# Performance work log

Hardware: AMD Instinct MI355X
Metric: run time of the kernel (lower is better)

Reference implementation:

```python
import jax, jax.numpy as jnp
import numpy as np

L, E, NH, V, BS = 8, 1024, 16, 32000, 1024  # layers, embed, heads, vocab, block_size
HD = E // NH  # head dim = 64
FF = 4 * E


def layernorm(x, scale, bias, eps=1e-5):
    mu = jnp.mean(x, axis=-1, keepdims=True)
    var = jnp.var(x, axis=-1, keepdims=True)
    return (x - mu) * jax.lax.rsqrt(var + eps) * scale + bias


def setup_inputs() -> dict:
    key = jax.random.key(0)
    ks = jax.random.split(key, 16)
    s = 0.02
    B, T = 2, 1024
    return {
        "idx": jax.random.randint(ks[0], (B, T), 0, V),
        "tok_emb": jax.random.normal(ks[1], (V, E), jnp.float32) * s,
        "pos_emb": jax.random.normal(ks[2], (BS, E), jnp.float32) * s,
        "Wq": jax.random.normal(ks[3], (L, E, E), jnp.float32) * s,
        "Wk": jax.random.normal(ks[4], (L, E, E), jnp.float32) * s,
        "Wv": jax.random.normal(ks[5], (L, E, E), jnp.float32) * s,
        "Wo": jax.random.normal(ks[6], (L, E, E), jnp.float32) * s,
        "bo": jnp.zeros((L, E), jnp.float32),
        "ln1_s": jnp.ones((L, E), jnp.float32),
        "ln1_b": jnp.zeros((L, E), jnp.float32),
        "W1": jax.random.normal(ks[7], (L, E, FF), jnp.float32) * s,
        "b1": jnp.zeros((L, FF), jnp.float32),
        "W2": jax.random.normal(ks[8], (L, FF, E), jnp.float32) * s,
        "b2": jnp.zeros((L, E), jnp.float32),
        "ln2_s": jnp.ones((L, E), jnp.float32),
        "ln2_b": jnp.zeros((L, E), jnp.float32),
        "lnf_s": jnp.ones((E,), jnp.float32),
        "lnf_b": jnp.zeros((E,), jnp.float32),
        "lm_w": jax.random.normal(ks[9], (E, V), jnp.float32) * s,
        "lm_b": jnp.zeros((V,), jnp.float32),
    }


def reference(idx, tok_emb, pos_emb, Wq, Wk, Wv, Wo, bo, ln1_s, ln1_b,
              W1, b1, W2, b2, ln2_s, ln2_b, lnf_s, lnf_b, lm_w, lm_b):
    B, T = idx.shape
    x = tok_emb[idx] + pos_emb[:T]  # [B,T,E]
    causal = jnp.triu(jnp.ones((T, T), bool), 1)  # True above diagonal -> masked
    scale = 1.0 / jnp.sqrt(jnp.asarray(HD, x.dtype))
    for l in range(L):
        h = layernorm(x, ln1_s[l], ln1_b[l])
        q = (h @ Wq[l]).reshape(B, T, NH, HD)
        k = (h @ Wk[l]).reshape(B, T, NH, HD)
        v = (h @ Wv[l]).reshape(B, T, NH, HD)
        scores = jnp.einsum("bthd,bshd->bhts", q, k) * scale  # [B,H,T,T]
        scores = jnp.where(causal, -jnp.inf, scores)
        attn = jax.nn.softmax(scores, axis=-1)
        o = jnp.einsum("bhts,bshd->bthd", attn, v).reshape(B, T, E)
        x = x + o @ Wo[l] + bo[l]
        h2 = layernorm(x, ln2_s[l], ln2_b[l])
        x = x + jax.nn.gelu(h2 @ W1[l] + b1[l], approximate=False) @ W2[l] + b2[l]
    x = layernorm(x, lnf_s, lnf_b)
    logits = x @ lm_w + lm_b  # [B,T,V]
    return logits
```

## Files before the change

### kernel.cpp

```cpp
#include <hip/hip_runtime.h>

#define EDIM 1024
#define NHEADS 16
#define HDIM 64
#define TSEQ 1024
#define NBATCH 2
#define MROWS 2048
#define FFDIM 4096
#define NLAYERS 8
#define VOCAB 32000
#define QKVN 3072
#define SC2 0.18033688011112042f

typedef __attribute__((ext_vector_type(4))) float f32x4;
typedef __attribute__((ext_vector_type(8))) short short8;

__device__ __forceinline__ unsigned short f2bf(float f) {
    union { float f; unsigned u; } v; v.f = f;
    unsigned r = v.u + 0x7fffu + ((v.u >> 16) & 1u);
    return (unsigned short)(r >> 16);
}

__device__ __forceinline__ f32x4 mfma_bf16(short8 a, short8 b, f32x4 c) {
    return __builtin_amdgcn_mfma_f32_16x16x32_bf16(a, b, c, 0, 0, 0);
}

__device__ __forceinline__ void gload16(const unsigned short* g, unsigned short* l) {
    __builtin_amdgcn_global_load_lds(
        (const __attribute__((address_space(1))) unsigned int*)g,
        (__attribute__((address_space(3))) unsigned int*)l, 16, 0, 0);
}

__global__ __launch_bounds__(256) void embed_kernel(
    const int* __restrict__ idx, const float* __restrict__ tok,
    const float* __restrict__ pos, float* __restrict__ x)
{
    int row = blockIdx.x;
    int t = row & (TSEQ - 1);
    int tokid = idx[row];
    const float* tp = tok + (size_t)tokid * EDIM;
    const float* pp = pos + (size_t)t * EDIM;
    float* xp = x + (size_t)row * EDIM;
    int c = threadIdx.x * 4;
    f32x4 a = *(const f32x4*)(tp + c);
    f32x4 b = *(const f32x4*)(pp + c);
    *(f32x4*)(xp + c) = a + b;
}

__device__ __forceinline__ void ln_store(
    f32x4 v, int tid, const float* __restrict__ sc, const float* __restrict__ bi,
    unsigned short* __restrict__ hrow)
{
    float sum = v[0] + v[1] + v[2] + v[3];
    float sq = v[0]*v[0] + v[1]*v[1] + v[2]*v[2] + v[3]*v[3];
    #pragma unroll
    for (int m = 1; m <= 32; m <<= 1) { sum += __shfl_xor(sum, m); sq += __shfl_xor(sq, m); }
    __shared__ float sh[8];
    int w = tid >> 6;
    if ((tid & 63) == 0) { sh[w] = sum; sh[4 + w] = sq; }
    __syncthreads();
    sum = sh[0] + sh[1] + sh[2] + sh[3];
    sq  = sh[4] + sh[5] + sh[6] + sh[7];
    float mu = sum * (1.0f / EDIM);
    float inv = rsqrtf(sq * (1.0f / EDIM) - mu * mu + 1e-5f);
    int c = tid * 4;
    unsigned o0 = (unsigned)f2bf((v[0] - mu) * inv * sc[c + 0] + bi[c + 0])
                | ((unsigned)f2bf((v[1] - mu) * inv * sc[c + 1] + bi[c + 1]) << 16);
    unsigned o1 = (unsigned)f2bf((v[2] - mu) * inv * sc[c + 2] + bi[c + 2])
                | ((unsigned)f2bf((v[3] - mu) * inv * sc[c + 3] + bi[c + 3]) << 16);
    unsigned* hp = (unsigned*)(hrow + c);
    hp[0] = o0; hp[1] = o1;
}

__global__ __launch_bounds__(256) void ln_kernel(
    const float* __restrict__ x, const float* __restrict__ sc,
    const float* __restrict__ bi, unsigned short* __restrict__ h)
{
    int row = blockIdx.x, tid = threadIdx.x;
    f32x4 v = *(const f32x4*)(x + (size_t)row * EDIM + tid * 4);
    ln_store(v, tid, sc, bi, h + (size_t)row * EDIM);
}

template<int KZ>
__global__ __launch_bounds__(256) void reduce_ln_kernel(
    const float* __restrict__ part, const float* __restrict__ bias,
    float* __restrict__ x, const float* __restrict__ sc,
    const float* __restrict__ bi, unsigned short* __restrict__ h)
{
    int row = blockIdx.x, tid = threadIdx.x;
    int c = tid * 4;
    f32x4 s = *(const f32x4*)(x + (size_t)row * EDIM + c);
    s += *(const f32x4*)(bias + c);
    #pragma unroll
    for (int kz = 0; kz < KZ; ++kz)
        s += *(const f32x4*)(part + ((size_t)kz * MROWS + row) * EDIM + c);
    *(f32x4*)(x + (size_t)row * EDIM + c) = s;
    ln_store(s, tid, sc, bi, h + (size_t)row * EDIM);
}

__device__ __forceinline__ void conv_tile(
    const float* __restrict__ W, unsigned short* __restrict__ WT,
    int Kdim, int Ndim, int k0, int n0, int tid)
{
    __shared__ unsigned short T[64][72];
    int r = tid >> 4, c4 = (tid & 15) * 4;
    #pragma unroll
    for (int i = 0; i < 4; ++i) {
        f32x4 v = *(const f32x4*)(W + (size_t)(k0 + r + 16 * i) * Ndim + n0 + c4);
        T[c4 + 0][r + 16 * i] = f2bf(v[0]);
        T[c4 + 1][r + 16 * i] = f2bf(v[1]);
        T[c4 + 2][r + 16 * i] = f2bf(v[2]);
        T[c4 + 3][r + 16 * i] = f2bf(v[3]);
    }
    __syncthreads();
    int nr = tid >> 2, kc = (tid & 3) * 16;
    short8 o0 = *(const short8*)&T[nr][kc];
    short8 o1 = *(const short8*)&T[nr][kc + 8];
    *(short8*)(WT + (size_t)(n0 + nr) * Kdim + k0 + kc)     = o0;
    *(short8*)(WT + (size_t)(n0 + nr) * Kdim + k0 + kc + 8) = o1;
}

__global__ __launch_bounds__(256) void wconv_layer_kernel(
    const float* __restrict__ Wq, const float* __restrict__ Wk,
    const float* __restrict__ Wv, const float* __restrict__ Wo,
    const float* __restrict__ W1, const float* __restrict__ W2,
    unsigned short* __restrict__ qkvT, unsigned short* __restrict__ woT,
    unsigned short* __restrict__ w1T, unsigned short* __restrict__ w2T)
{
    int bid = blockIdx.x, tid = threadIdx.x;
    if (bid < 768) {
        int wsel = bid >> 8, t = bid & 255;
        const float* src = wsel == 0 ? Wq : (wsel == 1 ? Wk : Wv);
        conv_tile(src, qkvT + (size_t)wsel * EDIM * EDIM, EDIM, EDIM,
                  (t & 15) * 64, (t >> 4) * 64, tid);
    } else if (bid < 1024) {
        int t = bid - 768;
        conv_tile(Wo, woT, EDIM, EDIM, (t & 15) * 64, (t >> 4) * 64, tid);
    } else if (bid < 2048) {
        int t = bid - 1024;
        conv_tile(W1, w1T, EDIM, FFDIM, (t & 15) * 64, (t >> 4) * 64, tid);
    } else {
        int t = bid - 2048;
        conv_tile(W2, w2T, FFDIM, EDIM, (t >> 4) * 64, (t & 15) * 64, tid);
    }
}

__global__ __launch_bounds__(256) void wconv_kernel(
    const float* __restrict__ W, unsigned short* __restrict__ WT, int Kdim, int Ndim)
{
    conv_tile(W, WT, Kdim, Ndim, blockIdx.x * 64, blockIdx.y * 64, threadIdx.x);
}

template<int EPI>
__global__ __launch_bounds__(256, 3) void gemm128(
    const unsigned short* __restrict__ A, const unsigned short* __restrict__ WT,
    const float* __restrict__ bias, float* __restrict__ Cf,
    unsigned short* __restrict__ Cb, int Ndim, int Kdim,
    int ntiles, int nwg, int kspan)
{
    __shared__ __align__(16) unsigned short A_lds[128][64];
    __shared__ __align__(16) unsigned short B_lds[128][64];
    int tid = threadIdx.x;
    int q8 = nwg >> 3;
    int swz = (int)(blockIdx.x & 7) * q8 + (int)(blockIdx.x >> 3);
    int bm0 = (swz / ntiles) * 128, bn0 = (swz % ntiles) * 128;
    int kz = blockIdx.y;
    int lane = tid & 63, w = tid >> 6;
    int wr = w >> 1, wc = w & 1;
    int r16 = lane & 15, cc = lane >> 4;
    int lrow = lane >> 3;
    int lcol = ((lane & 7) ^ lrow) * 8;
    int sw = r16 & 7;

    f32x4 acc[4][4];
    #pragma unroll
    for (int m = 0; m < 4; ++m)
        #pragma unroll
        for (int n = 0; n < 4; ++n) acc[m][n] = {0.f, 0.f, 0.f, 0.f};

    int kbeg = kz * kspan, kend = kbeg + kspan;
    for (int k0 = kbeg; k0 < kend; k0 += 64) {
        #pragma unroll
        for (int i = 0; i < 4; ++i) {
            int c = i * 4 + w;
            gload16(A + (size_t)(bm0 + c * 8 + lrow) * Kdim + k0 + lcol,
                    (unsigned short*)A_lds + c * 512);
            gload16(WT + (size_t)(bn0 + c * 8 + lrow) * Kdim + k0 + lcol,
                    (unsigned short*)B_lds + c * 512);
        }
        __syncthreads();
        #pragma unroll
        for (int kh = 0; kh < 2; ++kh) {
            short8 af[4], bfr[4];
            #pragma unroll
            for (int m = 0; m < 4; ++m)
                af[m] = *(const short8*)&A_lds[wr * 64 + m * 16 + r16][((kh * 4 + cc) ^ sw) * 8];
            #pragma unroll
            for (int n = 0; n < 4; ++n)
                bfr[n] = *(const short8*)&B_lds[wc * 64 + n * 16 + r16][((kh * 4 + cc) ^ sw) * 8];
            #pragma unroll
            for (int m = 0; m < 4; ++m)
                #pragma unroll
                for (int n = 0; n < 4; ++n)
                    acc[m][n] = mfma_bf16(af[m], bfr[n], acc[m][n]);
        }
        __syncthreads();
    }

    #pragma unroll
    for (int m = 0; m < 4; ++m) {
        #pragma unroll
        for (int n = 0; n < 4; ++n) {
            #pragma unroll
            for (int j = 0; j < 4; ++j) {
                int row = bm0 + wr * 64 + m * 16 + cc * 4 + j;
                int col = bn0 + wc * 64 + n * 16 + r16;
                float vv = acc[m][n][j];
                if constexpr (EPI == 0)
                    Cb[(size_t)row * Ndim + col] = f2bf(vv);
                else
                    (Cf + (size_t)kz * MROWS * Ndim)[(size_t)row * Ndim + col] = vv;
            }
        }
    }
}

template<int EPI>
__global__ __launch_bounds__(512, 2) void gemm_p3(
    const unsigned short* __restrict__ A, const unsigned short* __restrict__ WT,
    const float* __restrict__ bias, float* __restrict__ Cf,
    unsigned short* __restrict__ Cb, int Ndim, int Kdim, int mtiles, int ntiles)
{
    __shared__ __align__(16) unsigned short LDS[3][24576];
    const int tid = threadIdx.x;
    const int nwg = mtiles * ntiles, q8 = nwg >> 3;
    const int swz = (int)(blockIdx.x & 7) * q8 + (int)(blockIdx.x >> 3);
    const int bn0 = (swz / mtiles) * 256, bm0 = (swz % mtiles) * 128;
    const int lane = tid & 63, w = tid >> 6;
    const int wr = w >> 2, wc = w & 3;
    const int r16 = lane & 15, cc = lane >> 4;
    const int lrow = lane >> 3;
    const int lcol = ((lane & 7) ^ lrow) * 8;
    const int sw = r16 & 7;

    f32x4 acc[4][4];
    #pragma unroll
    for (int m = 0; m < 4; ++m)
        #pragma unroll
        for (int n = 0; n < 4; ++n) acc[m][n] = {0.f, 0.f, 0.f, 0.f};

    const int nk = Kdim >> 6;

    auto STAGE = [&](int t, int bufidx) {
        int k0 = t * 64;
        unsigned short* buf = &LDS[bufidx][0];
        #pragma unroll
        for (int i = 0; i < 2; ++i) {
            int c = i * 8 + w;
            gload16(A + (size_t)(bm0 + c * 8 + lrow) * Kdim + k0 + lcol, buf + c * 512);
        }
        #pragma unroll
        for (int i = 0; i < 4; ++i) {
            int c = i * 8 + w;
            gload16(WT + (size_t)(bn0 + c * 8 + lrow) * Kdim + k0 + lcol, buf + 8192 + c * 512);
        }
    };

    STAGE(0, 0);
    STAGE(1, 1);
    asm volatile("s_waitcnt vmcnt(6)" ::: "memory");
    __builtin_amdgcn_sched_barrier(0);
    __builtin_amdgcn_s_barrier();
    __builtin_amdgcn_sched_barrier(0);

    int cur = 0;
    for (int t = 0; t < nk; ++t) {
        if (t + 2 < nk) STAGE(t + 2, cur == 0 ? 2 : cur - 1);
        const unsigned short* Abuf = &LDS[cur][0];
        const unsigned short* Bbuf = &LDS[cur][8192];
        #pragma unroll
        for (int kh = 0; kh < 2; ++kh) {
            short8 af[4], bfr[4];
            #pragma unroll
            for (int m = 0; m < 4; ++m)
                af[m] = *(const short8*)&Abuf[(wr * 64 + m * 16 + r16) * 64 + ((kh * 4 + cc) ^ sw) * 8];
            #pragma unroll
            for (int n = 0; n < 4; ++n)
                bfr[n] = *(const short8*)&Bbuf[(wc * 64 + n * 16 + r16) * 64 + ((kh * 4 + cc) ^ sw) * 8];
            __builtin_amdgcn_s_setprio(1);
            #pragma unroll
            for (int m = 0; m < 4; ++m)
                #pragma unroll
                for (int n = 0; n < 4; ++n)
                    acc[m][n] = mfma_bf16(af[m], bfr[n], acc[m][n]);
            __builtin_amdgcn_s_setprio(0);
        }
        if (t + 1 < nk) {
            if (t + 2 < nk) asm volatile("s_waitcnt vmcnt(6)" ::: "memory");
            else            asm volatile("s_waitcnt vmcnt(0)" ::: "memory");
            __builtin_amdgcn_sched_barrier(0);
            __builtin_amdgcn_s_barrier();
            __builtin_amdgcn_sched_barrier(0);
            asm volatile("" ::: "memory");
        }
        cur = cur == 2 ? 0 : cur + 1;
    }

    #pragma unroll
    for (int m = 0; m < 4; ++m) {
        #pragma unroll
        for (int n = 0; n < 4; ++n) {
            #pragma unroll
            for (int j = 0; j < 4; ++j) {
                int row = bm0 + wr * 64 + m * 16 + cc * 4 + j;
                int col = bn0 + wc * 64 + n * 16 + r16;
                float vv = acc[m][n][j] + bias[col];
                if constexpr (EPI == 2) {
                    vv = 0.5f * vv * (1.0f + erff(vv * 0.70710678118654752f));
                    Cb[(size_t)row * Ndim + col] = f2bf(vv);
                } else {
                    Cf[(size_t)row * Ndim + col] = vv;
                }
            }
        }
    }
}

__global__ __launch_bounds__(256, 2) void gemm_wide_lm(
    const unsigned short* __restrict__ A, const unsigned short* __restrict__ WT,
    const float* __restrict__ bias, float* __restrict__ Cf,
    int Ndim, int Kdim, int mtiles, int ntiles)
{
    __shared__ __align__(16) unsigned short A_lds[128][64];
    __shared__ __align__(16) unsigned short B_lds[256][64];
    int tid = threadIdx.x;
    int nwg = mtiles * ntiles;
    int q8 = nwg >> 3;
    int swz = (int)(blockIdx.x & 7) * q8 + (int)(blockIdx.x >> 3);
    int bn0 = (swz / mtiles) * 256, bm0 = (swz % mtiles) * 128;
    int lane = tid & 63, w = tid >> 6;
    int wr = w >> 1, wc = w & 1;
    int r16 = lane & 15, cc = lane >> 4;
    int lrow = lane >> 3;
    int lcol = ((lane & 7) ^ lrow) * 8;
    int sw = r16 & 7;

    f32x4 acc[4][8];
    #pragma unroll
    for (int m = 0; m < 4; ++m)
        #pragma unroll
        for (int n = 0; n < 8; ++n) acc[m][n] = {0.f, 0.f, 0.f, 0.f};

    for (int k0 = 0; k0 < Kdim; k0 += 64) {
        #pragma unroll
        for (int i = 0; i < 4; ++i) {
            int c = i * 4 + w;
            gload16(A + (size_t)(bm0 + c * 8 + lrow) * Kdim + k0 + lcol,
                    (unsigned short*)A_lds + c * 512);
        }
        #pragma unroll
        for (int i = 0; i < 8; ++i) {
            int c = i * 4 + w;
            gload16(WT + (size_t)(bn0 + c * 8 + lrow) * Kdim + k0 + lcol,
                    (unsigned short*)B_lds + c * 512);
        }
        __syncthreads();
        #pragma unroll
        for (int kh = 0; kh < 2; ++kh) {
            short8 af[4], bfr[8];
            #pragma unroll
            for (int m = 0; m < 4; ++m)
                af[m] = *(const short8*)&A_lds[wr * 64 + m * 16 + r16][((kh * 4 + cc) ^ sw) * 8];
            #pragma unroll
            for (int n = 0; n < 8; ++n)
                bfr[n] = *(const short8*)&B_lds[wc * 128 + n * 16 + r16][((kh * 4 + cc) ^ sw) * 8];
            #pragma unroll
            for (int m = 0; m < 4; ++m)
                #pragma unroll
                for (int n = 0; n < 8; ++n)
                    acc[m][n] = mfma_bf16(af[m], bfr[n], acc[m][n]);
        }
        __syncthreads();
    }

    #pragma unroll
    for (int m = 0; m < 4; ++m) {
        #pragma unroll
        for (int n = 0; n < 8; ++n) {
            #pragma unroll
            for (int j = 0; j < 4; ++j) {
                int row = bm0 + wr * 64 + m * 16 + cc * 4 + j;
                int col = bn0 + wc * 128 + n * 16 + r16;
                Cf[(size_t)row * Ndim + col] = acc[m][n][j] + bias[col];
            }
        }
    }
}

__global__ __launch_bounds__(256) void attn_kernel(
    const unsigned short* __restrict__ qkv, unsigned short* __restrict__ o)
{
    __shared__ __align__(16) unsigned short K_lds[128][72];
    __shared__ __align__(16) unsigned short VT_lds[64][136];
    __shared__ __align__(16) unsigned short P_lds[4][16][136];

    int qt = blockIdx.x, head = blockIdx.y, bb = blockIdx.z;
    int tid = threadIdx.x, w = tid >> 6, lane = tid & 63;
    int r16 = lane & 15, cc = lane >> 4;
    size_t base = ((size_t)bb * TSEQ) * QKVN + head * HDIM;
    const unsigned short* q = qkv + base;
    const unsigned short* k = qkv + base + EDIM;
    const unsigned short* v = qkv + base + 2 * EDIM;
    size_t obase = ((size_t)bb * TSEQ) * EDIM + head * HDIM;
    int qbase = qt * 64;

    const unsigned short* qp = q + (size_t)(qbase + w * 16 + r16) * QKVN;
    short8 aq0 = *(const short8*)(qp + cc * 8);
    short8 aq1 = *(const short8*)(qp + 32 + cc * 8);

    f32x4 oacc[4];
    float m2[4], lrow[4];
    #pragma unroll
    for (int n = 0; n < 4; ++n) oacc[n] = {0.f, 0.f, 0.f, 0.f};
    #pragma unroll
    for (int j = 0; j < 4; ++j) { m2[j] = -1e30f; lrow[j] = 0.f; }

    int krow = tid >> 1, kch = (tid & 1) * 32;
    int vk2 = (tid & 63) * 2, vdb = (tid >> 6) * 16;

    int nkt = (qt + 2) >> 1;
    for (int kt = 0; kt < nkt; ++kt) {
        int kbase = kt * 128;
        const unsigned short* kp = k + (size_t)(kbase + krow) * QKVN + kch;
        *(short8*)&K_lds[krow][kch]      = *(const short8*)kp;
        *(short8*)&K_lds[krow][kch + 8]  = *(const short8*)(kp + 8);
        *(short8*)&K_lds[krow][kch + 16] = *(const short8*)(kp + 16);
        *(short8*)&K_lds[krow][kch + 24] = *(const short8*)(kp + 24);
        const unsigned short* vp0 = v + (size_t)(kbase + vk2) * QKVN + vdb;
        short8 v0a = *(const short8*)vp0;
        short8 v0b = *(const short8*)(vp0 + 8);
        short8 v1a = *(const short8*)(vp0 + QKVN);
        short8 v1b = *(const short8*)(vp0 + QKVN + 8);
        #pragma unroll
        for (int i = 0; i < 8; ++i) {
            *(unsigned*)&VT_lds[vdb + i][vk2] =
                (unsigned)(unsigned short)v0a[i] | ((unsigned)(unsigned short)v1a[i] << 16);
            *(unsigned*)&VT_lds[vdb + 8 + i][vk2] =
                (unsigned)(unsigned short)v0b[i] | ((unsigned)(unsigned short)v1b[i] << 16);
        }
        __syncthreads();

        f32x4 s[8];
        __builtin_amdgcn_s_setprio(1);
        #pragma unroll
        for (int n = 0; n < 8; ++n) {
            short8 bk0 = *(const short8*)&K_lds[n * 16 + r16][cc * 8];
            short8 bk1 = *(const short8*)&K_lds[n * 16 + r16][32 + cc * 8];
            f32x4 z = {0.f, 0.f, 0.f, 0.f};
            z = mfma_bf16(aq0, bk0, z);
            z = mfma_bf16(aq1, bk1, z);
            s[n] = z;
        }
        __builtin_amdgcn_s_setprio(0);
        int myrow = qbase + w * 16 + cc * 4;
        #pragma unroll
        for (int n = 0; n < 8; ++n) {
            int key = kbase + n * 16 + r16;
            #pragma unroll
            for (int j = 0; j < 4; ++j) {
                float sv = s[n][j] * SC2;
                if (key > myrow + j) sv = -1e30f;
                s[n][j] = sv;
            }
        }
        float tmax[4];
        #pragma unroll
        for (int j = 0; j < 4; ++j) {
            float t0 = fmaxf(fmaxf(s[0][j], s[1][j]), fmaxf(s[2][j], s[3][j]));
            float t1 = fmaxf(fmaxf(s[4][j], s[5][j]), fmaxf(s[6][j], s[7][j]));
            float tm = fmaxf(t0, t1);
            #pragma unroll
            for (int mm = 1; mm <= 8; mm <<= 1) tm = fmaxf(tm, __shfl_xor(tm, mm));
            tmax[j] = tm;
        }
        bool defer = (tmax[0] - m2[0] <= 11.5f) && (tmax[1] - m2[1] <= 11.5f)
                  && (tmax[2] - m2[2] <= 11.5f) && (tmax[3] - m2[3] <= 11.5f);
        if (!__all(defer)) {
            #pragma unroll
            for (int j = 0; j < 4; ++j) {
                float mnew = fmaxf(m2[j], tmax[j]);
                float al = exp2f(m2[j] - mnew);
                m2[j] = mnew;
                lrow[j] *= al;
                #pragma unroll
                for (int n = 0; n < 4; ++n) oacc[n][j] *= al;
            }
        }
        #pragma unroll
        for (int j = 0; j < 4; ++j) {
            float ts = 0.f;
            #pragma unroll
            for (int n = 0; n < 8; ++n) {
                float pe = exp2f(s[n][j] - m2[j]);
                s[n][j] = pe;
                ts += pe;
            }
            #pragma unroll
            for (int mm = 1; mm <= 8; mm <<= 1) ts += __shfl_xor(ts, mm);
            lrow[j] += ts;
        }
        #pragma unroll
        for (int n = 0; n < 8; ++n)
            #pragma unroll
            for (int j = 0; j < 4; ++j)
                P_lds[w][cc * 4 + j][n * 16 + r16] = f2bf(s[n][j]);
        short8 pa[4];
        #pragma unroll
        for (int qq = 0; qq < 4; ++qq)
            pa[qq] = *(const short8*)&P_lds[w][r16][qq * 32 + cc * 8];
        __builtin_amdgcn_s_setprio(1);
        #pragma unroll
        for (int n = 0; n < 4; ++n) {
            #pragma unroll
            for (int qq = 0; qq < 4; ++qq) {
                short8 bv = *(const short8*)&VT_lds[n * 16 + r16][qq * 32 + cc * 8];
                oacc[n] = mfma_bf16(pa[qq], bv, oacc[n]);
            }
        }
        __builtin_amdgcn_s_setprio(0);
        __syncthreads();
    }
    float rl[4];
    #pragma unroll
    for (int j = 0; j < 4; ++j) rl[j] = 1.0f / lrow[j];
    #pragma unroll
    for (int n = 0; n < 4; ++n)
        #pragma unroll
        for (int j = 0; j < 4; ++j) {
            int row = qbase + w * 16 + cc * 4 + j;
            o[obase + (size_t)row * EDIM + n * 16 + r16] = f2bf(oacc[n][j] * rl[j]);
        }
}

extern "C" void kernel_launch(void* const* d_in, const int* in_sizes, int n_in,
                              void* d_out, int out_size, void* d_ws, size_t ws_size,
                              hipStream_t stream) {
    const int*   idx     = (const int*)d_in[0];
    const float* tok_emb = (const float*)d_in[1];
    const float* pos_emb = (const float*)d_in[2];
    const float* Wq      = (const float*)d_in[3];
    const float* Wk      = (const float*)d_in[4];
    const float* Wv      = (const float*)d_in[5];
    const float* Wo      = (const float*)d_in[6];
    const float* bo      = (const float*)d_in[7];
    const float* ln1_s   = (const float*)d_in[8];
    const float* ln1_b   = (const float*)d_in[9];
    const float* W1      = (const float*)d_in[10];
    const float* b1      = (const float*)d_in[11];
    const float* W2      = (const float*)d_in[12];
    const float* b2      = (const float*)d_in[13];
    const float* ln2_s   = (const float*)d_in[14];
    const float* ln2_b   = (const float*)d_in[15];
    const float* lnf_s   = (const float*)d_in[16];
    const float* lnf_b   = (const float*)d_in[17];
    const float* lm_w    = (const float*)d_in[18];
    const float* lm_b    = (const float*)d_in[19];
    float* out = (float*)d_out;

    char* ws = (char*)d_ws;
    float*          x    = (float*)ws;
    unsigned short* h    = (unsigned short*)(ws + (8  << 20));
    unsigned short* qkv  = (unsigned short*)(ws + (12 << 20));
    unsigned short* ao   = (unsigned short*)(ws + (24 << 20));
    unsigned short* ff   = (unsigned short*)(ws + (28 << 20));
    unsigned short* qkvT = (unsigned short*)(ws + (44 << 20));
    unsigned short* woT  = (unsigned short*)(ws + (50 << 20));
    unsigned short* w1T  = (unsigned short*)(ws + (52 << 20));
    unsigned short* w2T  = (unsigned short*)(ws + (60 << 20));
    unsigned short* lmT  = (unsigned short*)(ws + (68 << 20));
    float*          part = (float*)(ws + (68 << 20));

    dim3 blk(256);
    embed_kernel<<<MROWS, blk, 0, stream>>>(idx, tok_emb, pos_emb, x);
    ln_kernel<<<MROWS, blk, 0, stream>>>(x, ln1_s, ln1_b, h);

    for (int l = 0; l < NLAYERS; ++l) {
        size_t eo = (size_t)l * EDIM * EDIM;
        wconv_layer_kernel<<<3072, blk, 0, stream>>>(
            Wq + eo, Wk + eo, Wv + eo, Wo + eo,
            W1 + (size_t)l * EDIM * FFDIM, W2 + (size_t)l * FFDIM * EDIM,
            qkvT, woT, w1T, w2T);

        gemm128<0><<<dim3(384, 1), blk, 0, stream>>>(h, qkvT, nullptr, nullptr, qkv, QKVN, EDIM, 24, 384, EDIM);
        attn_kernel<<<dim3(TSEQ / 64, NHEADS, NBATCH), blk, 0, stream>>>(qkv, ao);
        gemm128<4><<<dim3(128, 4), blk, 0, stream>>>(ao, woT, nullptr, part, nullptr, EDIM, EDIM, 8, 128, 256);
        reduce_ln_kernel<4><<<MROWS, blk, 0, stream>>>(part, bo + l * EDIM, x, ln2_s + l * EDIM, ln2_b + l * EDIM, h);
        gemm_p3<2><<<dim3(256, 1), dim3(512), 0, stream>>>(h, w1T, b1 + l * FFDIM, nullptr, ff, FFDIM, EDIM, 16, 16);
        gemm128<4><<<dim3(128, 4), blk, 0, stream>>>(ff, w2T, nullptr, part, nullptr, EDIM, FFDIM, 8, 128, 1024);
        if (l < NLAYERS - 1)
            reduce_ln_kernel<4><<<MROWS, blk, 0, stream>>>(part, b2 + l * EDIM, x, ln1_s + (l + 1) * EDIM, ln1_b + (l + 1) * EDIM, h);
        else
            reduce_ln_kernel<4><<<MROWS, blk, 0, stream>>>(part, b2 + l * EDIM, x, lnf_s, lnf_b, h);
    }
    wconv_kernel<<<dim3(16, 500), blk, 0, stream>>>(lm_w, lmT, EDIM, VOCAB);
    gemm_wide_lm<<<dim3(2000, 1), blk, 0, stream>>>(h, lmT, lm_b, out, VOCAB, EDIM, 16, 125);
}
```

Measured before the change: 1.521 ms.

## Overlap next-layer weight conversion with FF2 GEMM in fused kernel

Merges next-layer weight conversion (and, on the last layer, the LM-head weight conversion) into the FF2 GEMM launch as extra workgroups. The conversion work then fills idle compute units instead of running as a separate serial kernel. W2 is double-buffered so the weight in use is never overwritten. Also fuses embedding with the first layernorm and reverses the attention query-tile order so the longer causal tiles are scheduled first. This needs a larger workspace, checked at runtime, and falls back to the old path otherwise.

```diff
diff --git a/kernel.cpp b/kernel.cpp
--- a/kernel.cpp
+++ b/kernel.cpp
@@ -29,22 +29,6 @@
     __builtin_amdgcn_global_load_lds(
         (const __attribute__((address_space(1))) unsigned int*)g,
         (__attribute__((address_space(3))) unsigned int*)l, 16, 0, 0);
-}
-
-__global__ __launch_bounds__(256) void embed_kernel(
-    const int* __restrict__ idx, const float* __restrict__ tok,
-    const float* __restrict__ pos, float* __restrict__ x)
-{
-    int row = blockIdx.x;
-    int t = row & (TSEQ - 1);
-    int tokid = idx[row];
-    const float* tp = tok + (size_t)tokid * EDIM;
-    const float* pp = pos + (size_t)t * EDIM;
-    float* xp = x + (size_t)row * EDIM;
-    int c = threadIdx.x * 4;
-    f32x4 a = *(const f32x4*)(tp + c);
-    f32x4 b = *(const f32x4*)(pp + c);
-    *(f32x4*)(xp + c) = a + b;
 }
 
 __device__ __forceinline__ void ln_store(
@@ -72,12 +56,20 @@
     hp[0] = o0; hp[1] = o1;
 }
 
-__global__ __launch_bounds__(256) void ln_kernel(
-    const float* __restrict__ x, const float* __restrict__ sc,
-    const float* __restrict__ bi, unsigned short* __restrict__ h)
+__global__ __launch_bounds__(256) void embed_ln_kernel(
+    const int* __restrict__ idx, const float* __restrict__ tok,
+    const float* __restrict__ pos, float* __restrict__ x,
+    const float* __restrict__ sc, const float* __restrict__ bi,
+    unsigned short* __restrict__ h)
 {
     int row = blockIdx.x, tid = threadIdx.x;
-    f32x4 v = *(const f32x4*)(x + (size_t)row * EDIM + tid * 4);
+    int t = row & (TSEQ - 1);
+    int tokid = idx[row];
+    int c = tid * 4;
+    f32x4 a = *(const f32x4*)(tok + (size_t)tokid * EDIM + c);
+    f32x4 b = *(const f32x4*)(pos + (size_t)t * EDIM + c);
+    f32x4 v = a + b;
+    *(f32x4*)(x + (size_t)row * EDIM + c) = v;
     ln_store(v, tid, sc, bi, h + (size_t)row * EDIM);
 }
 
@@ -99,25 +91,49 @@
 }
 
 __device__ __forceinline__ void conv_tile(
+    unsigned short* __restrict__ Tb,
     const float* __restrict__ W, unsigned short* __restrict__ WT,
     int Kdim, int Ndim, int k0, int n0, int tid)
 {
-    __shared__ unsigned short T[64][72];
     int r = tid >> 4, c4 = (tid & 15) * 4;
     #pragma unroll
     for (int i = 0; i < 4; ++i) {
         f32x4 v = *(const f32x4*)(W + (size_t)(k0 + r + 16 * i) * Ndim + n0 + c4);
-        T[c4 + 0][r + 16 * i] = f2bf(v[0]);
-        T[c4 + 1][r + 16 * i] = f2bf(v[1]);
-        T[c4 + 2][r + 16 * i] = f2bf(v[2]);
-        T[c4 + 3][r + 16 * i] = f2bf(v[3]);
+        Tb[(c4 + 0) * 72 + r + 16 * i] = f2bf(v[0]);
+        Tb[(c4 + 1) * 72 + r + 16 * i] = f2bf(v[1]);
+        Tb[(c4 + 2) * 72 + r + 16 * i] = f2bf(v[2]);
+        Tb[(c4 + 3) * 72 + r + 16 * i] = f2bf(v[3]);
     }
     __syncthreads();
     int nr = tid >> 2, kc = (tid & 3) * 16;
-    short8 o0 = *(const short8*)&T[nr][kc];
-    short8 o1 = *(const short8*)&T[nr][kc + 8];
+    short8 o0 = *(const short8*)&Tb[nr * 72 + kc];
+    short8 o1 = *(const short8*)&Tb[nr * 72 + kc + 8];
     *(short8*)(WT + (size_t)(n0 + nr) * Kdim + k0 + kc)     = o0;
     *(short8*)(WT + (size_t)(n0 + nr) * Kdim + k0 + kc + 8) = o1;
+}
+
+__device__ __forceinline__ void wconv_layer_body(
+    unsigned short* Tb, int t, int tid,
+    const float* Wq, const float* Wk, const float* Wv, const float* Wo,
+    const float* W1, const float* W2,
+    unsigned short* qkvT, unsigned short* woT,
+    unsigned short* w1T, unsigned short* w2T)
+{
+    if (t < 768) {
+        int wsel = t >> 8, tt = t & 255;
+        const float* src = wsel == 0 ? Wq : (wsel == 1 ? Wk : Wv);
+        conv_tile(Tb, src, qkvT + (size_t)wsel * EDIM * EDIM, EDIM, EDIM,
+                  (tt & 15) * 64, (tt >> 4) * 64, tid);
+    } else if (t < 1024) {
+        int tt = t - 768;
+        conv_tile(Tb, Wo, woT, EDIM, EDIM, (tt & 15) * 64, (tt >> 4) * 64, tid);
+    } else if (t < 2048) {
+        int tt = t - 1024;
+        conv_tile(Tb, W1, w1T, EDIM, FFDIM, (tt & 15) * 64, (tt >> 4) * 64, tid);
+    } else {
+        int tt = t - 2048;
+        conv_tile(Tb, W2, w2T, FFDIM, EDIM, (tt >> 4) * 64, (tt & 15) * 64, tid);
+    }
 }
 
 __global__ __launch_bounds__(256) void wconv_layer_kernel(
@@ -127,44 +143,31 @@
     unsigned short* __restrict__ qkvT, unsigned short* __restrict__ woT,
     unsigned short* __restrict__ w1T, unsigned short* __restrict__ w2T)
 {
-    int bid = blockIdx.x, tid = threadIdx.x;
-    if (bid < 768) {
-        int wsel = bid >> 8, t = bid & 255;
-        const float* src = wsel == 0 ? Wq : (wsel == 1 ? Wk : Wv);
-        conv_tile(src, qkvT + (size_t)wsel * EDIM * EDIM, EDIM, EDIM,
-                  (t & 15) * 64, (t >> 4) * 64, tid);
-    } else if (bid < 1024) {
-        int t = bid - 768;
-        conv_tile(Wo, woT, EDIM, EDIM, (t & 15) * 64, (t >> 4) * 64, tid);
-    } else if (bid < 2048) {
-        int t = bid - 1024;
-        conv_tile(W1, w1T, EDIM, FFDIM, (t & 15) * 64, (t >> 4) * 64, tid);
-    } else {
-        int t = bid - 2048;
-        conv_tile(W2, w2T, FFDIM, EDIM, (t >> 4) * 64, (t & 15) * 64, tid);
-    }
+    __shared__ __align__(16) unsigned short Tb[64 * 72];
+    wconv_layer_body(Tb, blockIdx.x, threadIdx.x, Wq, Wk, Wv, Wo, W1, W2,
+                     qkvT, woT, w1T, w2T);
 }
 
 __global__ __launch_bounds__(256) void wconv_kernel(
     const float* __restrict__ W, unsigned short* __restrict__ WT, int Kdim, int Ndim)
 {
-    conv_tile(W, WT, Kdim, Ndim, blockIdx.x * 64, blockIdx.y * 64, threadIdx.x);
+    __shared__ __align__(16) unsigned short Tb[64 * 72];
+    conv_tile(Tb, W, WT, Kdim, Ndim, blockIdx.x * 64, blockIdx.y * 64, threadIdx.x);
 }
 
 template<int EPI>
-__global__ __launch_bounds__(256, 3) void gemm128(
+__device__ __forceinline__ void gemm128_body(
+    unsigned short* SMEM,
     const unsigned short* __restrict__ A, const unsigned short* __restrict__ WT,
-    const float* __restrict__ bias, float* __restrict__ Cf,
-    unsigned short* __restrict__ Cb, int Ndim, int Kdim,
-    int ntiles, int nwg, int kspan)
-{
-    __shared__ __align__(16) unsigned short A_lds[128][64];
-    __shared__ __align__(16) unsigned short B_lds[128][64];
+    float* __restrict__ Cf, unsigned short* __restrict__ Cb,
+    int Ndim, int Kdim, int ntiles, int nwg, int kspan, int bid, int kz)
+{
+    unsigned short* A_lds = SMEM;
+    unsigned short* B_lds = SMEM + 8192;
     int tid = threadIdx.x;
     int q8 = nwg >> 3;
-    int swz = (int)(blockIdx.x & 7) * q8 + (int)(blockIdx.x >> 3);
+    int swz = (bid & 7) * q8 + (bid >> 3);
     int bm0 = (swz / ntiles) * 128, bn0 = (swz % ntiles) * 128;
-    int kz = blockIdx.y;
     int lane = tid & 63, w = tid >> 6;
     int wr = w >> 1, wc = w & 1;
     int r16 = lane & 15, cc = lane >> 4;
@@ -183,10 +186,8 @@
         #pragma unroll
         for (int i = 0; i < 4; ++i) {
             int c = i * 4 + w;
-            gload16(A + (size_t)(bm0 + c * 8 + lrow) * Kdim + k0 + lcol,
-                    (unsigned short*)A_lds + c * 512);
-            gload16(WT + (size_t)(bn0 + c * 8 + lrow) * Kdim + k0 + lcol,
-                    (unsigned short*)B_lds + c * 512);
+            gload16(A + (size_t)(bm0 + c * 8 + lrow) * Kdim + k0 + lcol, A_lds + c * 512);
+            gload16(WT + (size_t)(bn0 + c * 8 + lrow) * Kdim + k0 + lcol, B_lds + c * 512);
         }
         __syncthreads();
         #pragma unroll
@@ -194,10 +195,10 @@
             short8 af[4], bfr[4];
             #pragma unroll
             for (int m = 0; m < 4; ++m)
-                af[m] = *(const short8*)&A_lds[wr * 64 + m * 16 + r16][((kh * 4 + cc) ^ sw) * 8];
+                af[m] = *(const short8*)&A_lds[(wr * 64 + m * 16 + r16) * 64 + ((kh * 4 + cc) ^ sw) * 8];
             #pragma unroll
             for (int n = 0; n < 4; ++n)
-                bfr[n] = *(const short8*)&B_lds[wc * 64 + n * 16 + r16][((kh * 4 + cc) ^ sw) * 8];
+                bfr[n] = *(const short8*)&B_lds[(wc * 64 + n * 16 + r16) * 64 + ((kh * 4 + cc) ^ sw) * 8];
             #pragma unroll
             for (int m = 0; m < 4; ++m)
                 #pragma unroll
@@ -222,6 +223,43 @@
                     (Cf + (size_t)kz * MROWS * Ndim)[(size_t)row * Ndim + col] = vv;
             }
         }
+    }
+}
+
+template<int EPI>
+__global__ __launch_bounds__(256, 3) void gemm128(
+    const unsigned short* __restrict__ A, const unsigned short* __restrict__ WT,
+    float* __restrict__ Cf, unsigned short* __restrict__ Cb,
+    int Ndim, int Kdim, int ntiles, int nwg, int kspan)
+{
+    __shared__ __align__(16) unsigned short SMEM[16384];
+    gemm128_body<EPI>(SMEM, A, WT, Cf, Cb, Ndim, Kdim, ntiles, nwg, kspan,
+                      blockIdx.x, blockIdx.y);
+}
+
+template<int MODE>
+__global__ __launch_bounds__(256, 3) void ff2_fused_kernel(
+    const unsigned short* __restrict__ A, const unsigned short* __restrict__ WT,
+    float* __restrict__ Cf,
+    const float* __restrict__ Wq, const float* __restrict__ Wk,
+    const float* __restrict__ Wv, const float* __restrict__ Wo,
+    const float* __restrict__ W1, const float* __restrict__ W2,
+    const float* __restrict__ lmW,
+    unsigned short* __restrict__ qkvT, unsigned short* __restrict__ woT,
+    unsigned short* __restrict__ w1T, unsigned short* __restrict__ w2Tn,
+    unsigned short* __restrict__ lmT)
+{
+    __shared__ __align__(16) unsigned short SMEM[16384];
+    int bid = blockIdx.x;
+    if (bid < 512) {
+        gemm128_body<4>(SMEM, A, WT, Cf, nullptr, EDIM, FFDIM, 8, 128, 1024,
+                        bid & 127, bid >> 7);
+    } else if constexpr (MODE == 0) {
+        wconv_layer_body(SMEM, bid - 512, threadIdx.x, Wq, Wk, Wv, Wo, W1, W2,
+                         qkvT, woT, w1T, w2Tn);
+    } else {
+        int t = bid - 512;
+        conv_tile(SMEM, lmW, lmT, EDIM, VOCAB, (t & 15) * 64, (t >> 4) * 64, threadIdx.x);
     }
 }
 
@@ -404,7 +442,8 @@
     __shared__ __align__(16) unsigned short VT_lds[64][136];
     __shared__ __align__(16) unsigned short P_lds[4][16][136];
 
-    int qt = blockIdx.x, head = blockIdx.y, bb = blockIdx.z;
+    int qt = (int)gridDim.x - 1 - (int)blockIdx.x;
+    int head = blockIdx.y, bb = blockIdx.z;
     int tid = threadIdx.x, w = tid >> 6, lane = tid & 63;
     int r16 = lane & 15, cc = lane >> 4;
     size_t base = ((size_t)bb * TSEQ) * QKVN + head * HDIM;
@@ -567,41 +606,68 @@
     const float* lm_b    = (const float*)d_in[19];
     float* out = (float*)d_out;
 
+    const size_t MB = 1 << 20;
     char* ws = (char*)d_ws;
     float*          x    = (float*)ws;
-    unsigned short* h    = (unsigned short*)(ws + (8  << 20));
-    unsigned short* qkv  = (unsigned short*)(ws + (12 << 20));
-    unsigned short* ao   = (unsigned short*)(ws + (24 << 20));
-    unsigned short* ff   = (unsigned short*)(ws + (28 << 20));
-    unsigned short* qkvT = (unsigned short*)(ws + (44 << 20));
-    unsigned short* woT  = (unsigned short*)(ws + (50 << 20));
-    unsigned short* w1T  = (unsigned short*)(ws + (52 << 20));
-    unsigned short* w2T  = (unsigned short*)(ws + (60 << 20));
-    unsigned short* lmT  = (unsigned short*)(ws + (68 << 20));
-    float*          part = (float*)(ws + (68 << 20));
+    unsigned short* h    = (unsigned short*)(ws + 8 * MB);
+    unsigned short* qkv  = (unsigned short*)(ws + 12 * MB);
+    unsigned short* ao   = (unsigned short*)(ws + 24 * MB);
+    unsigned short* ff   = (unsigned short*)(ws + 28 * MB);
+    unsigned short* qkvT = (unsigned short*)(ws + 44 * MB);
+    unsigned short* woT  = (unsigned short*)(ws + 50 * MB);
+    unsigned short* w1T  = (unsigned short*)(ws + 52 * MB);
+    unsigned short* w2Ta = (unsigned short*)(ws + 60 * MB);
+    unsigned short* lmT  = (unsigned short*)(ws + 68 * MB);
+
+    bool tier1 = ws_size >= (size_t)140 * MB;
+    bool tier2 = ws_size >= (size_t)172 * MB;
+    unsigned short* w2Tb = tier1 ? (unsigned short*)(ws + 131 * MB) : w2Ta;
+    float* part = (float*)(ws + (tier2 ? (size_t)139 * MB : (size_t)68 * MB));
 
     dim3 blk(256);
-    embed_kernel<<<MROWS, blk, 0, stream>>>(idx, tok_emb, pos_emb, x);
-    ln_kernel<<<MROWS, blk, 0, stream>>>(x, ln1_s, ln1_b, h);
+    embed_ln_kernel<<<MROWS, blk, 0, stream>>>(idx, tok_emb, pos_emb, x, ln1_s, ln1_b, h);
+    wconv_layer_kernel<<<3072, blk, 0, stream>>>(Wq, Wk, Wv, Wo, W1, W2,
+                                                 qkvT, woT, w1T, w2Ta);
 
     for (int l = 0; l < NLAYERS; ++l) {
-        size_t eo = (size_t)l * EDIM * EDIM;
-        wconv_layer_kernel<<<3072, blk, 0, stream>>>(
-            Wq + eo, Wk + eo, Wv + eo, Wo + eo,
-            W1 + (size_t)l * EDIM * FFDIM, W2 + (size_t)l * FFDIM * EDIM,
-            qkvT, woT, w1T, w2T);
-
-        gemm128<0><<<dim3(384, 1), blk, 0, stream>>>(h, qkvT, nullptr, nullptr, qkv, QKVN, EDIM, 24, 384, EDIM);
+        unsigned short* w2cur = (l & 1) ? w2Tb : w2Ta;
+        unsigned short* w2nxt = ((l + 1) & 1) ? w2Tb : w2Ta;
+        size_t eo1 = (size_t)(l + 1) * EDIM * EDIM;
+
+        gemm128<0><<<dim3(384, 1), blk, 0, stream>>>(h, qkvT, nullptr, qkv, QKVN, EDIM, 24, 384, EDIM);
         attn_kernel<<<dim3(TSEQ / 64, NHEADS, NBATCH), blk, 0, stream>>>(qkv, ao);
-        gemm128<4><<<dim3(128, 4), blk, 0, stream>>>(ao, woT, nullptr, part, nullptr, EDIM, EDIM, 8, 128, 256);
+        gemm128<4><<<dim3(128, 4), blk, 0, stream>>>(ao, woT, part, nullptr, EDIM, EDIM, 8, 128, 256);
         reduce_ln_kernel<4><<<MROWS, blk, 0, stream>>>(part, bo + l * EDIM, x, ln2_s + l * EDIM, ln2_b + l * EDIM, h);
         gemm_p3<2><<<dim3(256, 1), dim3(512), 0, stream>>>(h, w1T, b1 + l * FFDIM, nullptr, ff, FFDIM, EDIM, 16, 16);
-        gemm128<4><<<dim3(128, 4), blk, 0, stream>>>(ff, w2T, nullptr, part, nullptr, EDIM, FFDIM, 8, 128, 1024);
+        if (l < NLAYERS - 1) {
+            if (tier1)
+                ff2_fused_kernel<0><<<3584, blk, 0, stream>>>(
+                    ff, w2cur, part,
+                    Wq + eo1, Wk + eo1, Wv + eo1, Wo + eo1,
+                    W1 + (size_t)(l + 1) * EDIM * FFDIM, W2 + (size_t)(l + 1) * FFDIM * EDIM,
+                    nullptr, qkvT, woT, w1T, w2nxt, nullptr);
+            else {
+                gemm128<4><<<dim3(128, 4), blk, 0, stream>>>(ff, w2cur, part, nullptr, EDIM, FFDIM, 8, 128, 1024);
+                wconv_layer_kernel<<<3072, blk, 0, stream>>>(
+                    Wq + eo1, Wk + eo1, Wv + eo1, Wo + eo1,
+                    W1 + (size_t)(l + 1) * EDIM * FFDIM, W2 + (size_t)(l + 1) * FFDIM * EDIM,
+                    qkvT, woT, w1T, w2nxt);
+            }
+        } else {
+            if (tier2)
+                ff2_fused_kernel<1><<<8512, blk, 0, stream>>>(
+                    ff, w2cur, part,
+                    nullptr, nullptr, nullptr, nullptr, nullptr, nullptr,
+                    lm_w, nullptr, nullptr, nullptr, nullptr, lmT);
+            else
+                gemm128<4><<<dim3(128, 4), blk, 0, stream>>>(ff, w2cur, part, nullptr, EDIM, FFDIM, 8, 128, 1024);
+        }
         if (l < NLAYERS - 1)
             reduce_ln_kernel<4><<<MROWS, blk, 0, stream>>>(part, b2 + l * EDIM, x, ln1_s + (l + 1) * EDIM, ln1_b + (l + 1) * EDIM, h);
         else
             reduce_ln_kernel<4><<<MROWS, blk, 0, stream>>>(part, b2 + l * EDIM, x, lnf_s, lnf_b, h);
     }
-    wconv_kernel<<<dim3(16, 500), blk, 0, stream>>>(lm_w, lmT, EDIM, VOCAB);
+    if (!tier2)
+        wconv_kernel<<<dim3(16, 500), blk, 0, stream>>>(lm_w, lmT, EDIM, VOCAB);
     gemm_wide_lm<<<dim3(2000, 1), blk, 0, stream>>>(h, lmT, lm_b, out, VOCAB, EDIM, 16, 125);
 }
```

New measurement: 1.455 ms. 1.05x faster.
